# Optimization experiments

Measured on AMD Instinct MI355X. Metric: run time of the kernel, lower is better.

Reference implementation:

```python
import jax, jax.numpy as jnp
import numpy as np
from functools import partial

N_QUBITS = 8
DEPTH = 2
INPUT_DIM = 128
HIDDEN_DIM = N_QUBITS  # required: hx = o * tanh(cx) elementwise
DIM = 2 ** N_QUBITS

# Z expectation matrix: ZMAT[k, i] = +1/-1 depending on bit of basis state k at wire i
# (wire 0 is the most-significant qubit, PennyLane convention)
_bits = ((np.arange(DIM)[:, None] >> (N_QUBITS - 1 - np.arange(N_QUBITS)[None, :])) & 1)
ZMAT = jnp.asarray(1.0 - 2.0 * _bits, dtype=jnp.float32)  # [2**n, n]


def _apply_1q(state, G, wire):
    """Apply 2x2 gate G ([2,2] shared or [B,2,2] batched) on `wire`."""
    B = state.shape[0]
    left, right = 2 ** wire, 2 ** (N_QUBITS - wire - 1)
    s = state.reshape(B, left, 2, right)
    if G.ndim == 2:
        s = jnp.einsum('ij,bljr->blir', G, s)
    else:
        s = jnp.einsum('bij,bljr->blir', G, s)
    return s.reshape(B, DIM)


def _apply_cnot(state, wire):
    """CNOT with control=wire, target=wire+1 (adjacent)."""
    B = state.shape[0]
    left, right = 2 ** wire, 2 ** (N_QUBITS - wire - 2)
    s = state.reshape(B, left, 2, 2, right)
    s = jnp.concatenate([s[:, :, :1], s[:, :, 1:, ::-1]], axis=2)
    return s.reshape(B, DIM)


def quantum_gate(angles, params):
    """angles: [B, n] RX rotation angles; params: [depth, n] RY angles.
    Returns [B, n] PauliZ expectations (exact statevector simulation)."""
    B = angles.shape[0]
    state = jnp.zeros((B, DIM), dtype=jnp.complex64).at[:, 0].set(1.0)
    # RX encoding layer (batched angles)
    c = jnp.cos(angles / 2).astype(jnp.complex64)
    s = (-1j) * jnp.sin(angles / 2).astype(jnp.complex64)
    for i in range(N_QUBITS):
        G = jnp.stack([jnp.stack([c[:, i], s[:, i]], -1),
                       jnp.stack([s[:, i], c[:, i]], -1)], -2)  # [B,2,2]
        state = _apply_1q(state, G, i)
    # variational layers: RY (shared params) + CNOT chain
    cp = jnp.cos(params / 2).astype(jnp.complex64)
    sp = jnp.sin(params / 2).astype(jnp.complex64)
    for d in range(DEPTH):
        for i in range(N_QUBITS):
            G = jnp.array([[1.0, 0.0], [0.0, 1.0]], jnp.complex64)
            G = jnp.stack([jnp.stack([cp[d, i], -sp[d, i]]),
                           jnp.stack([sp[d, i], cp[d, i]])])  # [2,2]
            state = _apply_1q(state, G, i)
        for i in range(N_QUBITS - 1):
            state = _apply_cnot(state, i)
    probs = (state.real ** 2 + state.imag ** 2)  # [B, 2**n]
    return probs @ ZMAT  # [B, n]


def setup_inputs() -> dict:
    key = jax.random.key(0)
    ks = jax.random.split(key, 13)
    T, B = 256, 1024
    cat = INPUT_DIM + HIDDEN_DIM
    lin_scale = 1.0 / np.sqrt(cat)
    d = {'inputs': jax.random.normal(ks[0], (T, B, INPUT_DIM), jnp.float32)}
    for idx, g in enumerate(['f', 'i', 'g', 'o']):
        d[f'W{g}'] = jax.random.uniform(ks[1 + 3 * idx], (N_QUBITS, cat), jnp.float32, -lin_scale, lin_scale)
        d[f'b{g}'] = jax.random.uniform(ks[2 + 3 * idx], (N_QUBITS,), jnp.float32, -lin_scale, lin_scale)
        d[f'P{g}'] = jax.random.normal(ks[3 + 3 * idx], (DEPTH, N_QUBITS), jnp.float32)
    return d


def reference(inputs, Wf, bf, Pf, Wi, bi, Pi, Wg, bg, Pg, Wo, bo, Po):
    T, B, _ = inputs.shape
    h0 = jnp.zeros((B, HIDDEN_DIM), inputs.dtype)
    c0 = jnp.zeros((B, HIDDEN_DIM), inputs.dtype)

    def step(carry, x):
        hx, cx = carry
        comb = jnp.concatenate([x, hx], axis=1)  # [B, input+hidden]
        f = jax.nn.sigmoid(quantum_gate(comb @ Wf.T + bf, Pf))
        i = jax.nn.sigmoid(quantum_gate(comb @ Wi.T + bi, Pi))
        g = jnp.tanh(quantum_gate(comb @ Wg.T + bg, Pg))
        o = jax.nn.sigmoid(quantum_gate(comb @ Wo.T + bo, Po))
        cx = f * cx + i * g
        hx = o * jnp.tanh(cx)
        return (hx, cx), hx

    (hx, cx), outputs = jax.lax.scan(step, (h0, c0), inputs)
    return outputs, (hx, cx)
```

## Files before the change

### kernel.cpp

```cpp
#include <hip/hip_runtime.h>
#include <math.h>

#define TS 256
#define BB 1024
#define NQ 8
#define INDIM 128
#define CATDIM 136
#define INV2PI 0.15915494309189535f
#define LOG2E  1.4426950408889634f

typedef float v2f __attribute__((ext_vector_type(2)));
typedef __fp16 v2h __attribute__((ext_vector_type(2)));

__device__ __forceinline__ float dpp_xor1(float v) {
    return __int_as_float(__builtin_amdgcn_mov_dpp(__float_as_int(v), 0xB1, 0xF, 0xF, true));
}
__device__ __forceinline__ float dpp_xor2(float v) {
    return __int_as_float(__builtin_amdgcn_mov_dpp(__float_as_int(v), 0x4E, 0xF, 0xF, true));
}
__device__ __forceinline__ float dpp_xor8(float v) {
    return __int_as_float(__builtin_amdgcn_mov_dpp(__float_as_int(v), 0x128, 0xF, 0xF, true));
}
__device__ __forceinline__ float swz4(float v)  {
    return __int_as_float(__builtin_amdgcn_ds_swizzle(__float_as_int(v), 0x101F));
}
__device__ __forceinline__ float swz16(float v) {
    return __int_as_float(__builtin_amdgcn_ds_swizzle(__float_as_int(v), 0x401F));
}
__device__ __forceinline__ float swz20(float v) {
    return __int_as_float(__builtin_amdgcn_ds_swizzle(__float_as_int(v), 0x501F));
}
__device__ __forceinline__ float hw_sin(float x) { float r; asm("v_sin_f32 %0, %1" : "=v"(r) : "v"(x)); return r; }
__device__ __forceinline__ float hw_cos(float x) { float r; asm("v_cos_f32 %0, %1" : "=v"(r) : "v"(x)); return r; }
__device__ __forceinline__ float hw_exp(float x) { float r; asm("v_exp_f32 %0, %1" : "=v"(r) : "v"(x)); return r; }
__device__ __forceinline__ float hw_rcp(float x) { float r; asm("v_rcp_f32 %0, %1" : "=v"(r) : "v"(x)); return r; }
__device__ __forceinline__ v2f mk2(float x, float y) { v2f r; r.x = x; r.y = y; return r; }
__device__ __forceinline__ v2f pk_fma(v2f a, v2f b, v2f c) {
    v2f d; asm("v_pk_fma_f32 %0, %1, %2, %3" : "=v"(d) : "v"(a), "v"(b), "v"(c)); return d;
}
__device__ __forceinline__ float fdot2(v2h a, v2h b, float c) {
    float d; asm("v_dot2_f32_f16 %0, %1, %2, %3" : "=v"(d) : "v"(a), "v"(b), "v"(c)); return d;
}

__launch_bounds__(64, 1)
__attribute__((amdgpu_waves_per_eu(1, 1)))
__global__ void qlstm_f(const float* __restrict__ x,
    const float* __restrict__ Wf, const float* __restrict__ bf, const float* __restrict__ Pf,
    const float* __restrict__ Wi, const float* __restrict__ bi, const float* __restrict__ Pi,
    const float* __restrict__ Wg, const float* __restrict__ bg, const float* __restrict__ Pg,
    const float* __restrict__ Wo, const float* __restrict__ bo, const float* __restrict__ Po,
    float* __restrict__ out, float* __restrict__ hst, float* __restrict__ cst)
{
    const int lane = threadIdx.x;
    const int l0 = lane & 1, l1 = (lane >> 1) & 1, l3 = (lane >> 3) & 1;
    const int q = 4 * l0 + 2 * l1 + l3;
    const int g = ((lane >> 2) & 1) | ((lane >> 3) & 2);
    const int k1 = lane >> 5;
    const int b = blockIdx.x;
    const int c = 8 * k1 + q;

    const float* W; const float* P; const float* bs;
    if (g == 0)      { W = Wf; P = Pf; bs = bf; }
    else if (g == 1) { W = Wi; P = Pi; bs = bi; }
    else if (g == 2) { W = Wg; P = Pg; bs = bg; }
    else             { W = Wo; P = Po; bs = bo; }

    float Chw[8], nSw[8], hsp0[8], cp0c[8];
    #pragma unroll
    for (int w = 0; w < 8; ++w) {
        float s1, c1, s0, c0;
        __sincosf(P[8 + w], &s1, &c1);
        __sincosf(P[w], &s0, &c0);
        Chw[w] = 0.5f * c1;
        nSw[w] = -s1;
        hsp0[w] = 0.5f * s0;
        cp0c[w] = c0;
    }

    v2h xw[8][4];
    #pragma unroll
    for (int j = 0; j < 8; ++j) {
        const float* Wj = W + j * CATDIM + 8 * c;
        #pragma unroll
        for (int p2 = 0; p2 < 4; ++p2)
            xw[j][p2] = __builtin_amdgcn_cvt_pkrtz(INV2PI * Wj[2*p2], INV2PI * Wj[2*p2+1]);
    }

    v2f whq[4];
    {
        const float* Wq = W + q * CATDIM + INDIM;
        #pragma unroll
        for (int p2 = 0; p2 < 4; ++p2)
            whq[p2] = mk2(INV2PI * Wq[q ^ (2 * p2)], INV2PI * Wq[q ^ (2 * p2 + 1)]);
    }
    const float bq = INV2PI * bs[q];

    const float kl = ((g == 2) ? 2.f : -1.f) * LOG2E;
    const float Aa = (g == 2) ? 1.f : 0.f;
    const float Bb = (g == 2) ? -1.f : 1.f;
    float sel[8];
    #pragma unroll
    for (int i = 0; i < 8; ++i) sel[i] = (q == i) ? kl : 0.f;

    float s0h = 0.f, s1h = 0.f, s2h = 0.f, s3h = 0.f;
    float s4h = 0.f, s5h = 0.f, s6h = 0.f, s7h = 0.f;
    float c_own = 0.f, hv = 0.f;

    const float* xptr = x + (size_t)b * INDIM + 8 * c;
    v2h xh[4];
    {
        float4 a0 = *(const float4*)(xptr);
        float4 a1 = *(const float4*)(xptr + 4);
        xh[0] = __builtin_amdgcn_cvt_pkrtz(a0.x, a0.y);
        xh[1] = __builtin_amdgcn_cvt_pkrtz(a0.z, a0.w);
        xh[2] = __builtin_amdgcn_cvt_pkrtz(a1.x, a1.y);
        xh[3] = __builtin_amdgcn_cvt_pkrtz(a1.z, a1.w);
    }
    xptr += (size_t)BB * INDIM;

    const bool emit = (lane & 0x34) == 0;
    float* optr = out + (size_t)b * NQ + q;

    for (int t = 0; t < TS; ++t) {
        float pt[8];
        #pragma unroll
        for (int j = 0; j < 8; ++j) {
            float acc = fdot2(xh[0], xw[j][0], 0.f);
            acc = fdot2(xh[1], xw[j][1], acc);
            acc = fdot2(xh[2], xw[j][2], acc);
            acc = fdot2(xh[3], xw[j][3], acc);
            pt[j] = acc;
        }

        {
            float4 a0 = *(const float4*)(xptr);
            float4 a1 = *(const float4*)(xptr + 4);
            xptr += (t < TS - 2) ? (size_t)BB * INDIM : 0;
            xh[0] = __builtin_amdgcn_cvt_pkrtz(a0.x, a0.y);
            xh[1] = __builtin_amdgcn_cvt_pkrtz(a0.z, a0.w);
            xh[2] = __builtin_amdgcn_cvt_pkrtz(a1.x, a1.y);
            xh[3] = __builtin_amdgcn_cvt_pkrtz(a1.z, a1.w);
        }

        {
            float s, r;
            s = l0 ? pt[0] : pt[4]; r = dpp_xor1(s); pt[0] = (l0 ? pt[4] : pt[0]) + r;
            s = l0 ? pt[1] : pt[5]; r = dpp_xor1(s); pt[1] = (l0 ? pt[5] : pt[1]) + r;
            s = l0 ? pt[2] : pt[6]; r = dpp_xor1(s); pt[2] = (l0 ? pt[6] : pt[2]) + r;
            s = l0 ? pt[3] : pt[7]; r = dpp_xor1(s); pt[3] = (l0 ? pt[7] : pt[3]) + r;
            s = l1 ? pt[0] : pt[2]; r = dpp_xor2(s); pt[0] = (l1 ? pt[2] : pt[0]) + r;
            s = l1 ? pt[1] : pt[3]; r = dpp_xor2(s); pt[1] = (l1 ? pt[3] : pt[1]) + r;
            s = l3 ? pt[0] : pt[1]; r = dpp_xor8(s); pt[0] = (l3 ? pt[1] : pt[0]) + r;
            pt[0] += __shfl_xor(pt[0], 32, 64);
        }

        v2f hacc = pk_fma(mk2(s0h, s1h), whq[0], mk2(pt[0] + bq, 0.f));
        hacc = pk_fma(mk2(s2h, s3h), whq[1], hacc);
        hacc = pk_fma(mk2(s4h, s5h), whq[2], hacc);
        hacc = pk_fma(mk2(s6h, s7h), whq[3], hacc);
        float ang = hacc.x + hacc.y;

        float sa_own = hw_sin(ang);
        float ca_own = hw_cos(ang);

        float sa_0, sa_1, ca_0, ca_1;
        {
            float p = dpp_xor1(sa_own);
            sa_0 = l0 ? p : sa_own;  sa_1 = l0 ? sa_own : p;
            p = dpp_xor1(ca_own);
            ca_0 = l0 ? p : ca_own;  ca_1 = l0 ? ca_own : p;
        }
        float sa00, sa01, sa10, sa11, ca00, ca01, ca10, ca11;
        {
            float p0 = dpp_xor2(sa_0), p1 = dpp_xor2(sa_1);
            sa00 = l1 ? p0 : sa_0;  sa01 = l1 ? sa_0 : p0;
            sa10 = l1 ? p1 : sa_1;  sa11 = l1 ? sa_1 : p1;
            p0 = dpp_xor2(ca_0); p1 = dpp_xor2(ca_1);
            ca00 = l1 ? p0 : ca_0;  ca01 = l1 ? ca_0 : p0;
            ca10 = l1 ? p1 : ca_1;  ca11 = l1 ? ca_1 : p1;
        }
        float saw[8], caw[8];
        {
            float p;
            p = dpp_xor8(sa00); saw[0] = l3 ? p : sa00; saw[1] = l3 ? sa00 : p;
            p = dpp_xor8(sa01); saw[2] = l3 ? p : sa01; saw[3] = l3 ? sa01 : p;
            p = dpp_xor8(sa10); saw[4] = l3 ? p : sa10; saw[5] = l3 ? sa10 : p;
            p = dpp_xor8(sa11); saw[6] = l3 ? p : sa11; saw[7] = l3 ? sa11 : p;
            p = dpp_xor8(ca00); caw[0] = l3 ? p : ca00; caw[1] = l3 ? ca00 : p;
            p = dpp_xor8(ca01); caw[2] = l3 ? p : ca01; caw[3] = l3 ? ca01 : p;
            p = dpp_xor8(ca10); caw[4] = l3 ? p : ca10; caw[5] = l3 ? ca10 : p;
            p = dpp_xor8(ca11); caw[6] = l3 ? p : ca11; caw[7] = l3 ? ca11 : p;
        }

        float kE = 0.f;
        float d0, d1, zr, zi;
        {
            float AmB = cp0c[0] * caw[0];
            d0 = Chw[0] * (1.f + AmB);
            d1 = -(Chw[0] * (1.f - AmB));
            zr = nSw[0] * (hsp0[0] * caw[0]);
            zi = nSw[0] * (-0.5f * saw[0]);
        }
        #pragma unroll
        for (int w = 1; w < 8; ++w) {
            float gr = hsp0[w] * caw[w];
            float gi = -0.5f * saw[w];
            float AmB = cp0c[w] * caw[w];
            float sum = d0 + d1, dif = d0 - d1;
            float p = gr * zr, qv = gi * zi;
            float Ew = fmaf(4.f, p, sum);
            kE = fmaf(sel[w - 1], Ew, kE);
            float ad = AmB * dif;
            float e1 = sum + ad, e3 = sum - ad;
            float e2 = p - qv, e4 = p + qv;
            float T0 = fmaf(4.f, e2, e1);
            float T1 = fmaf(4.f, e4, e3);
            float f1 = fmaf(gr, sum, zr);
            float f3 = fmaf(AmB, zi, gi * dif);
            d0 = Chw[w] * T0;
            d1 = -(Chw[w] * T1);
            zr = nSw[w] * f1;
            zi = nSw[w] * f3;
        }
        {
            float E7 = (d0 + d1) + 2.f * zr;
            kE = fmaf(sel[7], E7, kE);
        }

        float y = hw_exp(kE);
        float a = fmaf(Aa, y, Bb) * hw_rcp(y + 1.f);

        float b4 = swz4(a);
        float b16 = swz16(a);
        float b20 = swz20(a);
        bool g1b = (g & 2) != 0;
        bool g0b = (g & 1) != 0;
        float e0 = g1b ? b16 : a;
        float e1s = g1b ? b20 : b4;
        float e2s = g1b ? a : b16;
        float e3s = g1b ? b4 : b20;
        float fv = g0b ? e1s : e0;
        float iv = g0b ? e0 : e1s;
        float gv = g0b ? e3s : e2s;
        float ov = g0b ? e2s : e3s;

        c_own = fmaf(fv, c_own, iv * gv);
        float e2c = hw_exp(c_own * (2.f * LOG2E));
        hv = ov * ((e2c - 1.f) * hw_rcp(e2c + 1.f));

        if (emit) *optr = hv;
        optr += (size_t)BB * NQ;

        s0h = hv;
        s4h = dpp_xor1(s0h);
        s2h = dpp_xor2(s0h);
        s6h = dpp_xor2(s4h);
        s1h = dpp_xor8(s0h);
        s5h = dpp_xor8(s4h);
        s3h = dpp_xor8(s2h);
        s7h = dpp_xor8(s6h);
    }

    if (emit) {
        hst[b * NQ + q] = hv;
        cst[b * NQ + q] = c_own;
    }
}

extern "C" void kernel_launch(void* const* d_in, const int* in_sizes, int n_in,
                              void* d_out, int out_size, void* d_ws, size_t ws_size,
                              hipStream_t stream) {
    const float* x  = (const float*)d_in[0];
    const float* Wf = (const float*)d_in[1];
    const float* bf = (const float*)d_in[2];
    const float* Pf = (const float*)d_in[3];
    const float* Wi = (const float*)d_in[4];
    const float* bi = (const float*)d_in[5];
    const float* Pi = (const float*)d_in[6];
    const float* Wg = (const float*)d_in[7];
    const float* bg = (const float*)d_in[8];
    const float* Pg = (const float*)d_in[9];
    const float* Wo = (const float*)d_in[10];
    const float* bo = (const float*)d_in[11];
    const float* Po = (const float*)d_in[12];

    float* out = (float*)d_out;
    float* hst = out + (size_t)TS * BB * NQ;
    float* cst = hst + (size_t)BB * NQ;

    qlstm_f<<<BB, 64, 0, stream>>>(x, Wf, bf, Pf, Wi, bi, Pi,
                                   Wg, bg, Pg, Wo, bo, Po,
                                   out, hst, cst);
}
```

Before: 236.6 us.

## Split into producer wave computing input projections and consumer wave running recurrence

The kernel now launches two waves per block. Wave 0 computes the x·W input projections for chunks of 32 timesteps in fp32 and stores them in shared memory. Wave 1 runs the serial quantum-LSTM recurrence, reading the precomputed projections, so the input GEMV and the global x loads are taken off the critical recurrent path. The cost is a block-wide barrier every chunk, a 32KB shared buffer, two waves per block instead of one, and fp32 math where packed fp16 dot products were used before.

Result: no change. 238.9 us (+1.0%).

```diff
diff --git a/kernel.cpp b/kernel.cpp
--- a/kernel.cpp
+++ b/kernel.cpp
@@ -8,9 +8,9 @@
 #define CATDIM 136
 #define INV2PI 0.15915494309189535f
 #define LOG2E  1.4426950408889634f
+#define CHUNK 32
 
 typedef float v2f __attribute__((ext_vector_type(2)));
-typedef __fp16 v2h __attribute__((ext_vector_type(2)));
 
 __device__ __forceinline__ float dpp_xor1(float v) {
     return __int_as_float(__builtin_amdgcn_mov_dpp(__float_as_int(v), 0xB1, 0xF, 0xF, true));
@@ -38,227 +38,221 @@
 __device__ __forceinline__ v2f pk_fma(v2f a, v2f b, v2f c) {
     v2f d; asm("v_pk_fma_f32 %0, %1, %2, %3" : "=v"(d) : "v"(a), "v"(b), "v"(c)); return d;
 }
-__device__ __forceinline__ float fdot2(v2h a, v2h b, float c) {
-    float d; asm("v_dot2_f32_f16 %0, %1, %2, %3" : "=v"(d) : "v"(a), "v"(b), "v"(c)); return d;
-}
-
-__launch_bounds__(64, 1)
-__attribute__((amdgpu_waves_per_eu(1, 1)))
-__global__ void qlstm_f(const float* __restrict__ x,
+
+__launch_bounds__(128, 1)
+__global__ void qlstm_pc(const float* __restrict__ x,
     const float* __restrict__ Wf, const float* __restrict__ bf, const float* __restrict__ Pf,
     const float* __restrict__ Wi, const float* __restrict__ bi, const float* __restrict__ Pi,
     const float* __restrict__ Wg, const float* __restrict__ bg, const float* __restrict__ Pg,
     const float* __restrict__ Wo, const float* __restrict__ bo, const float* __restrict__ Po,
     float* __restrict__ out, float* __restrict__ hst, float* __restrict__ cst)
 {
-    const int lane = threadIdx.x;
+    const int tid = threadIdx.x;
+    const int wv = tid >> 6;
+    const int lane = tid & 63;
+    const int b = blockIdx.x;
+
+    __shared__ float xp[TS * 32];
+
+    const float* Wlist[4] = { Wf, Wi, Wg, Wo };
+    const float* blist[4] = { bf, bi, bg, bo };
+    const float* Plist[4] = { Pf, Pi, Pg, Po };
+
     const int l0 = lane & 1, l1 = (lane >> 1) & 1, l3 = (lane >> 3) & 1;
     const int q = 4 * l0 + 2 * l1 + l3;
     const int g = ((lane >> 2) & 1) | ((lane >> 3) & 2);
-    const int k1 = lane >> 5;
-    const int b = blockIdx.x;
-    const int c = 8 * k1 + q;
-
-    const float* W; const float* P; const float* bs;
-    if (g == 0)      { W = Wf; P = Pf; bs = bf; }
-    else if (g == 1) { W = Wi; P = Pi; bs = bi; }
-    else if (g == 2) { W = Wg; P = Pg; bs = bg; }
-    else             { W = Wo; P = Po; bs = bo; }
 
     float Chw[8], nSw[8], hsp0[8], cp0c[8];
-    #pragma unroll
-    for (int w = 0; w < 8; ++w) {
-        float s1, c1, s0, c0;
-        __sincosf(P[8 + w], &s1, &c1);
-        __sincosf(P[w], &s0, &c0);
-        Chw[w] = 0.5f * c1;
-        nSw[w] = -s1;
-        hsp0[w] = 0.5f * s0;
-        cp0c[w] = c0;
-    }
-
-    v2h xw[8][4];
-    #pragma unroll
-    for (int j = 0; j < 8; ++j) {
-        const float* Wj = W + j * CATDIM + 8 * c;
-        #pragma unroll
-        for (int p2 = 0; p2 < 4; ++p2)
-            xw[j][p2] = __builtin_amdgcn_cvt_pkrtz(INV2PI * Wj[2*p2], INV2PI * Wj[2*p2+1]);
-    }
-
     v2f whq[4];
-    {
-        const float* Wq = W + q * CATDIM + INDIM;
+    float sel[8];
+    float kl = 0.f, Aa = 0.f, Bb = 0.f;
+    if (wv == 1) {
+        const float* P = Plist[g];
+        #pragma unroll
+        for (int w = 0; w < 8; ++w) {
+            float s1, c1, s0, c0;
+            __sincosf(P[8 + w], &s1, &c1);
+            __sincosf(P[w], &s0, &c0);
+            Chw[w] = 0.5f * c1;
+            nSw[w] = -s1;
+            hsp0[w] = 0.5f * s0;
+            cp0c[w] = c0;
+        }
+        const float* Wq = Wlist[g] + q * CATDIM + INDIM;
         #pragma unroll
         for (int p2 = 0; p2 < 4; ++p2)
             whq[p2] = mk2(INV2PI * Wq[q ^ (2 * p2)], INV2PI * Wq[q ^ (2 * p2 + 1)]);
+        kl = ((g == 2) ? 2.f : -1.f) * LOG2E;
+        Aa = (g == 2) ? 1.f : 0.f;
+        Bb = (g == 2) ? -1.f : 1.f;
+        #pragma unroll
+        for (int i = 0; i < 8; ++i) sel[i] = (q == i) ? kl : 0.f;
     }
-    const float bq = INV2PI * bs[q];
-
-    const float kl = ((g == 2) ? 2.f : -1.f) * LOG2E;
-    const float Aa = (g == 2) ? 1.f : 0.f;
-    const float Bb = (g == 2) ? -1.f : 1.f;
-    float sel[8];
-    #pragma unroll
-    for (int i = 0; i < 8; ++i) sel[i] = (q == i) ? kl : 0.f;
 
     float s0h = 0.f, s1h = 0.f, s2h = 0.f, s3h = 0.f;
     float s4h = 0.f, s5h = 0.f, s6h = 0.f, s7h = 0.f;
     float c_own = 0.f, hv = 0.f;
-
-    const float* xptr = x + (size_t)b * INDIM + 8 * c;
-    v2h xh[4];
-    {
-        float4 a0 = *(const float4*)(xptr);
-        float4 a1 = *(const float4*)(xptr + 4);
-        xh[0] = __builtin_amdgcn_cvt_pkrtz(a0.x, a0.y);
-        xh[1] = __builtin_amdgcn_cvt_pkrtz(a0.z, a0.w);
-        xh[2] = __builtin_amdgcn_cvt_pkrtz(a1.x, a1.y);
-        xh[3] = __builtin_amdgcn_cvt_pkrtz(a1.z, a1.w);
-    }
-    xptr += (size_t)BB * INDIM;
-
-    const bool emit = (lane & 0x34) == 0;
+    const bool emit = (wv == 1) && ((lane & 0x34) == 0);
     float* optr = out + (size_t)b * NQ + q;
 
-    for (int t = 0; t < TS; ++t) {
-        float pt[8];
-        #pragma unroll
-        for (int j = 0; j < 8; ++j) {
-            float acc = fdot2(xh[0], xw[j][0], 0.f);
-            acc = fdot2(xh[1], xw[j][1], acc);
-            acc = fdot2(xh[2], xw[j][2], acc);
-            acc = fdot2(xh[3], xw[j][3], acc);
-            pt[j] = acc;
-        }
-
-        {
-            float4 a0 = *(const float4*)(xptr);
-            float4 a1 = *(const float4*)(xptr + 4);
-            xptr += (t < TS - 2) ? (size_t)BB * INDIM : 0;
-            xh[0] = __builtin_amdgcn_cvt_pkrtz(a0.x, a0.y);
-            xh[1] = __builtin_amdgcn_cvt_pkrtz(a0.z, a0.w);
-            xh[2] = __builtin_amdgcn_cvt_pkrtz(a1.x, a1.y);
-            xh[3] = __builtin_amdgcn_cvt_pkrtz(a1.z, a1.w);
-        }
-
-        {
-            float s, r;
-            s = l0 ? pt[0] : pt[4]; r = dpp_xor1(s); pt[0] = (l0 ? pt[4] : pt[0]) + r;
-            s = l0 ? pt[1] : pt[5]; r = dpp_xor1(s); pt[1] = (l0 ? pt[5] : pt[1]) + r;
-            s = l0 ? pt[2] : pt[6]; r = dpp_xor1(s); pt[2] = (l0 ? pt[6] : pt[2]) + r;
-            s = l0 ? pt[3] : pt[7]; r = dpp_xor1(s); pt[3] = (l0 ? pt[7] : pt[3]) + r;
-            s = l1 ? pt[0] : pt[2]; r = dpp_xor2(s); pt[0] = (l1 ? pt[2] : pt[0]) + r;
-            s = l1 ? pt[1] : pt[3]; r = dpp_xor2(s); pt[1] = (l1 ? pt[3] : pt[1]) + r;
-            s = l3 ? pt[0] : pt[1]; r = dpp_xor8(s); pt[0] = (l3 ? pt[1] : pt[0]) + r;
-            pt[0] += __shfl_xor(pt[0], 32, 64);
-        }
-
-        v2f hacc = pk_fma(mk2(s0h, s1h), whq[0], mk2(pt[0] + bq, 0.f));
-        hacc = pk_fma(mk2(s2h, s3h), whq[1], hacc);
-        hacc = pk_fma(mk2(s4h, s5h), whq[2], hacc);
-        hacc = pk_fma(mk2(s6h, s7h), whq[3], hacc);
-        float ang = hacc.x + hacc.y;
-
-        float sa_own = hw_sin(ang);
-        float ca_own = hw_cos(ang);
-
-        float sa_0, sa_1, ca_0, ca_1;
-        {
-            float p = dpp_xor1(sa_own);
-            sa_0 = l0 ? p : sa_own;  sa_1 = l0 ? sa_own : p;
-            p = dpp_xor1(ca_own);
-            ca_0 = l0 ? p : ca_own;  ca_1 = l0 ? ca_own : p;
-        }
-        float sa00, sa01, sa10, sa11, ca00, ca01, ca10, ca11;
-        {
-            float p0 = dpp_xor2(sa_0), p1 = dpp_xor2(sa_1);
-            sa00 = l1 ? p0 : sa_0;  sa01 = l1 ? sa_0 : p0;
-            sa10 = l1 ? p1 : sa_1;  sa11 = l1 ? sa_1 : p1;
-            p0 = dpp_xor2(ca_0); p1 = dpp_xor2(ca_1);
-            ca00 = l1 ? p0 : ca_0;  ca01 = l1 ? ca_0 : p0;
-            ca10 = l1 ? p1 : ca_1;  ca11 = l1 ? ca_1 : p1;
-        }
-        float saw[8], caw[8];
-        {
-            float p;
-            p = dpp_xor8(sa00); saw[0] = l3 ? p : sa00; saw[1] = l3 ? sa00 : p;
-            p = dpp_xor8(sa01); saw[2] = l3 ? p : sa01; saw[3] = l3 ? sa01 : p;
-            p = dpp_xor8(sa10); saw[4] = l3 ? p : sa10; saw[5] = l3 ? sa10 : p;
-            p = dpp_xor8(sa11); saw[6] = l3 ? p : sa11; saw[7] = l3 ? sa11 : p;
-            p = dpp_xor8(ca00); caw[0] = l3 ? p : ca00; caw[1] = l3 ? ca00 : p;
-            p = dpp_xor8(ca01); caw[2] = l3 ? p : ca01; caw[3] = l3 ? ca01 : p;
-            p = dpp_xor8(ca10); caw[4] = l3 ? p : ca10; caw[5] = l3 ? ca10 : p;
-            p = dpp_xor8(ca11); caw[6] = l3 ? p : ca11; caw[7] = l3 ? ca11 : p;
-        }
-
-        float kE = 0.f;
-        float d0, d1, zr, zi;
-        {
-            float AmB = cp0c[0] * caw[0];
-            d0 = Chw[0] * (1.f + AmB);
-            d1 = -(Chw[0] * (1.f - AmB));
-            zr = nSw[0] * (hsp0[0] * caw[0]);
-            zi = nSw[0] * (-0.5f * saw[0]);
-        }
-        #pragma unroll
-        for (int w = 1; w < 8; ++w) {
-            float gr = hsp0[w] * caw[w];
-            float gi = -0.5f * saw[w];
-            float AmB = cp0c[w] * caw[w];
-            float sum = d0 + d1, dif = d0 - d1;
-            float p = gr * zr, qv = gi * zi;
-            float Ew = fmaf(4.f, p, sum);
-            kE = fmaf(sel[w - 1], Ew, kE);
-            float ad = AmB * dif;
-            float e1 = sum + ad, e3 = sum - ad;
-            float e2 = p - qv, e4 = p + qv;
-            float T0 = fmaf(4.f, e2, e1);
-            float T1 = fmaf(4.f, e4, e3);
-            float f1 = fmaf(gr, sum, zr);
-            float f3 = fmaf(AmB, zi, gi * dif);
-            d0 = Chw[w] * T0;
-            d1 = -(Chw[w] * T1);
-            zr = nSw[w] * f1;
-            zi = nSw[w] * f3;
-        }
-        {
-            float E7 = (d0 + d1) + 2.f * zr;
-            kE = fmaf(sel[7], E7, kE);
-        }
-
-        float y = hw_exp(kE);
-        float a = fmaf(Aa, y, Bb) * hw_rcp(y + 1.f);
-
-        float b4 = swz4(a);
-        float b16 = swz16(a);
-        float b20 = swz20(a);
-        bool g1b = (g & 2) != 0;
-        bool g0b = (g & 1) != 0;
-        float e0 = g1b ? b16 : a;
-        float e1s = g1b ? b20 : b4;
-        float e2s = g1b ? a : b16;
-        float e3s = g1b ? b4 : b20;
-        float fv = g0b ? e1s : e0;
-        float iv = g0b ? e0 : e1s;
-        float gv = g0b ? e3s : e2s;
-        float ov = g0b ? e2s : e3s;
-
-        c_own = fmaf(fv, c_own, iv * gv);
-        float e2c = hw_exp(c_own * (2.f * LOG2E));
-        hv = ov * ((e2c - 1.f) * hw_rcp(e2c + 1.f));
-
-        if (emit) *optr = hv;
-        optr += (size_t)BB * NQ;
-
-        s0h = hv;
-        s4h = dpp_xor1(s0h);
-        s2h = dpp_xor2(s0h);
-        s6h = dpp_xor2(s4h);
-        s1h = dpp_xor8(s0h);
-        s5h = dpp_xor8(s4h);
-        s3h = dpp_xor8(s2h);
-        s7h = dpp_xor8(s6h);
+    const int pq = lane >> 3;
+    const int kg = lane & 7;
+
+    auto fill_chunk = [&](int base) {
+        float4 wfrag[4][4];
+        float bias_w[4];
+        #pragma unroll
+        for (int g4 = 0; g4 < 4; ++g4) {
+            const float* Wr = Wlist[g4] + pq * CATDIM + kg * 16;
+            #pragma unroll
+            for (int c4 = 0; c4 < 4; ++c4) {
+                float4 v = *(const float4*)(Wr + c4 * 4);
+                v.x *= INV2PI; v.y *= INV2PI; v.z *= INV2PI; v.w *= INV2PI;
+                wfrag[g4][c4] = v;
+            }
+            bias_w[g4] = blist[g4][pq] * INV2PI;
+        }
+        for (int tt = 0; tt < CHUNK; ++tt) {
+            const int t = base + tt;
+            const float* xr = x + ((size_t)t * BB + b) * INDIM + kg * 16;
+            float4 x0 = *(const float4*)(xr);
+            float4 x1 = *(const float4*)(xr + 4);
+            float4 x2 = *(const float4*)(xr + 8);
+            float4 x3 = *(const float4*)(xr + 12);
+            #pragma unroll
+            for (int g4 = 0; g4 < 4; ++g4) {
+                float p =
+                    x0.x*wfrag[g4][0].x + x0.y*wfrag[g4][0].y + x0.z*wfrag[g4][0].z + x0.w*wfrag[g4][0].w +
+                    x1.x*wfrag[g4][1].x + x1.y*wfrag[g4][1].y + x1.z*wfrag[g4][1].z + x1.w*wfrag[g4][1].w +
+                    x2.x*wfrag[g4][2].x + x2.y*wfrag[g4][2].y + x2.z*wfrag[g4][2].z + x2.w*wfrag[g4][2].w +
+                    x3.x*wfrag[g4][3].x + x3.y*wfrag[g4][3].y + x3.z*wfrag[g4][3].z + x3.w*wfrag[g4][3].w;
+                p += dpp_xor1(p);
+                p += dpp_xor2(p);
+                p += __shfl_xor(p, 4, 64);
+                if (kg == 0) xp[t * 32 + g4 * 8 + pq] = p + bias_w[g4];
+            }
+        }
+    };
+
+    if (wv == 0) fill_chunk(0);
+    __syncthreads();
+
+    for (int k = 0; k < TS / CHUNK; ++k) {
+        if (wv == 0) {
+            if (k + 1 < TS / CHUNK) fill_chunk((k + 1) * CHUNK);
+        } else {
+            const int tbase = k * CHUNK;
+            for (int tt = 0; tt < CHUNK; ++tt) {
+                const int t = tbase + tt;
+                float xb = xp[t * 32 + g * 8 + q];
+                v2f hacc = pk_fma(mk2(s0h, s1h), whq[0], mk2(xb, 0.f));
+                hacc = pk_fma(mk2(s2h, s3h), whq[1], hacc);
+                hacc = pk_fma(mk2(s4h, s5h), whq[2], hacc);
+                hacc = pk_fma(mk2(s6h, s7h), whq[3], hacc);
+                float ang = hacc.x + hacc.y;
+
+                float sa_own = hw_sin(ang);
+                float ca_own = hw_cos(ang);
+
+                float sa_0, sa_1, ca_0, ca_1;
+                {
+                    float p = dpp_xor1(sa_own);
+                    sa_0 = l0 ? p : sa_own;  sa_1 = l0 ? sa_own : p;
+                    p = dpp_xor1(ca_own);
+                    ca_0 = l0 ? p : ca_own;  ca_1 = l0 ? ca_own : p;
+                }
+                float sa00, sa01, sa10, sa11, ca00, ca01, ca10, ca11;
+                {
+                    float p0 = dpp_xor2(sa_0), p1 = dpp_xor2(sa_1);
+                    sa00 = l1 ? p0 : sa_0;  sa01 = l1 ? sa_0 : p0;
+                    sa10 = l1 ? p1 : sa_1;  sa11 = l1 ? sa_1 : p1;
+                    p0 = dpp_xor2(ca_0); p1 = dpp_xor2(ca_1);
+                    ca00 = l1 ? p0 : ca_0;  ca01 = l1 ? ca_0 : p0;
+                    ca10 = l1 ? p1 : ca_1;  ca11 = l1 ? ca_1 : p1;
+                }
+                float saw[8], caw[8];
+                {
+                    float p;
+                    p = dpp_xor8(sa00); saw[0] = l3 ? p : sa00; saw[1] = l3 ? sa00 : p;
+                    p = dpp_xor8(sa01); saw[2] = l3 ? p : sa01; saw[3] = l3 ? sa01 : p;
+                    p = dpp_xor8(sa10); saw[4] = l3 ? p : sa10; saw[5] = l3 ? sa10 : p;
+                    p = dpp_xor8(sa11); saw[6] = l3 ? p : sa11; saw[7] = l3 ? sa11 : p;
+                    p = dpp_xor8(ca00); caw[0] = l3 ? p : ca00; caw[1] = l3 ? ca00 : p;
+                    p = dpp_xor8(ca01); caw[2] = l3 ? p : ca01; caw[3] = l3 ? ca01 : p;
+                    p = dpp_xor8(ca10); caw[4] = l3 ? p : ca10; caw[5] = l3 ? ca10 : p;
+                    p = dpp_xor8(ca11); caw[6] = l3 ? p : ca11; caw[7] = l3 ? ca11 : p;
+                }
+
+                float kE = 0.f;
+                float d0, d1, zr, zi;
+                {
+                    float AmB = cp0c[0] * caw[0];
+                    d0 = Chw[0] * (1.f + AmB);
+                    d1 = -(Chw[0] * (1.f - AmB));
+                    zr = nSw[0] * (hsp0[0] * caw[0]);
+                    zi = nSw[0] * (-0.5f * saw[0]);
+                }
+                #pragma unroll
+                for (int w = 1; w < 8; ++w) {
+                    float gr = hsp0[w] * caw[w];
+                    float gi = -0.5f * saw[w];
+                    float AmB = cp0c[w] * caw[w];
+                    float sum = d0 + d1, dif = d0 - d1;
+                    float p = gr * zr, qv = gi * zi;
+                    float Ew = fmaf(4.f, p, sum);
+                    kE = fmaf(sel[w - 1], Ew, kE);
+                    float ad = AmB * dif;
+                    float e1 = sum + ad, e3 = sum - ad;
+                    float e2 = p - qv, e4 = p + qv;
+                    float T0 = fmaf(4.f, e2, e1);
+                    float T1 = fmaf(4.f, e4, e3);
+                    float f1 = fmaf(gr, sum, zr);
+                    float f3 = fmaf(AmB, zi, gi * dif);
+                    d0 = Chw[w] * T0;
+                    d1 = -(Chw[w] * T1);
+                    zr = nSw[w] * f1;
+                    zi = nSw[w] * f3;
+                }
+                {
+                    float E7 = (d0 + d1) + 2.f * zr;
+                    kE = fmaf(sel[7], E7, kE);
+                }
+
+                float y = hw_exp(kE);
+                float a = fmaf(Aa, y, Bb) * hw_rcp(y + 1.f);
+
+                float b4 = swz4(a);
+                float b16 = swz16(a);
+                float b20 = swz20(a);
+                bool g1b = (g & 2) != 0;
+                bool g0b = (g & 1) != 0;
+                float e0 = g1b ? b16 : a;
+                float e1s = g1b ? b20 : b4;
+                float e2s = g1b ? a : b16;
+                float e3s = g1b ? b4 : b20;
+                float fv = g0b ? e1s : e0;
+                float iv = g0b ? e0 : e1s;
+                float gv = g0b ? e3s : e2s;
+                float ov = g0b ? e2s : e3s;
+
+                c_own = fmaf(fv, c_own, iv * gv);
+                float e2c = hw_exp(c_own * (2.f * LOG2E));
+                hv = ov * ((e2c - 1.f) * hw_rcp(e2c + 1.f));
+
+                if (emit) *optr = hv;
+                optr += (size_t)BB * NQ;
+
+                s0h = hv;
+                s4h = dpp_xor1(s0h);
+                s2h = dpp_xor2(s0h);
+                s6h = dpp_xor2(s4h);
+                s1h = dpp_xor8(s0h);
+                s5h = dpp_xor8(s4h);
+                s3h = dpp_xor8(s2h);
+                s7h = dpp_xor8(s6h);
+            }
+        }
+        __syncthreads();
     }
 
     if (emit) {
@@ -288,7 +282,7 @@
     float* hst = out + (size_t)TS * BB * NQ;
     float* cst = hst + (size_t)BB * NQ;
 
-    qlstm_f<<<BB, 64, 0, stream>>>(x, Wf, bf, Pf, Wi, bi, Pi,
-                                   Wg, bg, Pg, Wo, bo, Po,
-                                   out, hst, cst);
-}
+    qlstm_pc<<<BB, 128, 0, stream>>>(x, Wf, bf, Pf, Wi, bi, Pi,
+                                     Wg, bg, Pg, Wo, bo, Po,
+                                     out, hst, cst);
+}
```
